# Performance work log

Hardware: AMD Instinct MI355X
Metric: run time of the kernel (lower is better)

## Reference

```python
import jax, jax.numpy as jnp
import numpy as np

N_EMBD = 1024
N_HEAD = 16
LATENT = 64
HEAD_DIM = N_EMBD // N_HEAD
B, T = 2, 2048
SCALE = 1.0 / np.sqrt(LATENT)


def setup_inputs() -> dict:
    key = jax.random.key(0)
    ks = jax.random.split(key, 10)
    s = lambda fan_in: 1.0 / np.sqrt(fan_in)
    return {
        "x": jax.random.normal(ks[0], (B, T, N_EMBD), dtype=jnp.float32),
        "Wq": jax.random.normal(ks[1], (N_EMBD, N_EMBD), dtype=jnp.float32) * s(N_EMBD),
        "bq": jnp.zeros((N_EMBD,), dtype=jnp.float32),
        "Wk": jax.random.normal(ks[2], (N_EMBD, N_HEAD * LATENT), dtype=jnp.float32) * s(N_EMBD),
        "bk": jnp.zeros((N_HEAD * LATENT,), dtype=jnp.float32),
        "Wv": jax.random.normal(ks[3], (N_EMBD, N_HEAD * LATENT), dtype=jnp.float32) * s(N_EMBD),
        "bv": jnp.zeros((N_HEAD * LATENT,), dtype=jnp.float32),
        "Wo": jax.random.normal(ks[4], (N_HEAD * LATENT, N_EMBD), dtype=jnp.float32) * s(N_HEAD * LATENT),
        "bo": jnp.zeros((N_EMBD,), dtype=jnp.float32),
        "Wc": jax.random.normal(ks[5], (HEAD_DIM, LATENT), dtype=jnp.float32) * s(HEAD_DIM),
    }


def reference(x, Wq, bq, Wk, bk, Wv, bv, Wo, bo, Wc):
    Bv, Tv, C = x.shape
    # projections
    q = (x @ Wq + bq).reshape(Bv, Tv, N_HEAD, HEAD_DIM)        # [B,T,H,Dh]
    k = (x @ Wk + bk).reshape(Bv, Tv, N_HEAD, LATENT)          # [B,T,H,L]
    v = (x @ Wv + bv).reshape(Bv, Tv, N_HEAD, LATENT)          # [B,T,H,L]
    # compress q into latent dim: [B,T,H,L]
    qc = jnp.einsum("bthd,dl->bthl", q, Wc)
    # attention scores [B,H,T,T]
    att = jnp.einsum("bthl,bshl->bhts", qc, k) * SCALE
    causal = jnp.tril(jnp.ones((Tv, Tv), dtype=bool))
    att = jnp.where(causal[None, None], att, -jnp.inf)
    att = jax.nn.softmax(att, axis=-1)
    y = jnp.einsum("bhts,bshl->bthl", att, v).reshape(Bv, Tv, N_HEAD * LATENT)
    return y @ Wo + bo
```

## Files before the change

kernel.cpp:

```cpp
#include <hip/hip_runtime.h>
#include <stdint.h>

#define TT 2048
#define BB 2
#define MROWS (BB*TT)
#define LSCALE 0.18033688011112043f

typedef unsigned short u16;
typedef __bf16 bf16x8 __attribute__((ext_vector_type(8)));
typedef float f32x4 __attribute__((ext_vector_type(4)));
typedef short s16x8 __attribute__((ext_vector_type(8)));
typedef unsigned short u16x4 __attribute__((ext_vector_type(4)));

#define GLOBAL_AS const __attribute__((address_space(1))) void*
#define LDS_AS __attribute__((address_space(3))) void*

__device__ __forceinline__ u16 f2b(float f){
  uint32_t u = __builtin_bit_cast(uint32_t, f);
  u = (u + 0x7FFFu + ((u >> 16) & 1u)) >> 16;
  return (u16)u;
}
__device__ __forceinline__ float b2f(u16 u){
  return __builtin_bit_cast(float, (uint32_t)u << 16);
}

__global__ __launch_bounds__(256) void prep(
    const float* __restrict__ x, const float* __restrict__ Wq,
    const float* __restrict__ Wc, const float* __restrict__ bq,
    const float* __restrict__ Wk, const float* __restrict__ Wv,
    const float* __restrict__ Wo,
    u16* __restrict__ xb, u16* __restrict__ WqcT, u16* __restrict__ WkT,
    u16* __restrict__ WvT, u16* __restrict__ WoT, float* __restrict__ bqc){
  const int i = blockIdx.x, t = threadIdx.x;
  if (i < 4096){
    int id = i * 256 + t;
    float4 v = ((const float4*)x)[id];
    u16x4 o; o.x = f2b(v.x); o.y = f2b(v.y); o.z = f2b(v.z); o.w = f2b(v.w);
    ((u16x4*)xb)[id] = o;
    return;
  }
  if (i < 7168){
    int j = i - 4096;
    int z = j >> 10, rem = j & 1023;
    const float* in = (z == 0) ? Wk : (z == 1) ? Wv : Wo;
    u16* out = (z == 0) ? WkT : (z == 1) ? WvT : WoT;
    __shared__ float tl[32][33];
    int tx = t & 31, ty = t >> 5;
    int c0 = (rem & 31) * 32, r0 = (rem >> 5) * 32;
    #pragma unroll
    for (int k = 0; k < 32; k += 8)
      tl[ty + k][tx] = in[(size_t)(r0 + ty + k) * 1024 + c0 + tx];
    __syncthreads();
    #pragma unroll
    for (int k = 0; k < 32; k += 8)
      out[(size_t)(c0 + ty + k) * 1024 + r0 + tx] = f2b(tl[tx][ty + k]);
    return;
  }
  __shared__ float wc[4096];
  #pragma unroll
  for (int k = 0; k < 16; ++k) wc[k * 256 + t] = Wc[k * 256 + t];
  __syncthreads();
  if (i == 7424){
    #pragma unroll
    for (int k = 0; k < 4; ++k){
      int nn = t * 4 + k;
      int h = nn >> 6, lc = nn & 63;
      float a = 0.f;
      #pragma unroll
      for (int dd = 0; dd < 64; ++dd) a += bq[h * 64 + dd] * wc[dd * 64 + lc];
      bqc[nn] = a;
    }
    return;
  }
  __shared__ float tile[64][65];
  const int j = i - 7168;
  const int db = j >> 4, hb = j & 15;
  {
    int dl = t >> 2, lq = t & 3;
    const float4* wq4 = (const float4*)(Wq + (size_t)(db * 64 + dl) * 1024 + hb * 64);
    float wqr[64];
    #pragma unroll
    for (int k = 0; k < 16; ++k){
      float4 v = wq4[k];
      wqr[k * 4] = v.x; wqr[k * 4 + 1] = v.y; wqr[k * 4 + 2] = v.z; wqr[k * 4 + 3] = v.w;
    }
    #pragma unroll
    for (int jj = 0; jj < 16; ++jj){
      int lc = lq * 16 + jj;
      float a = 0.f;
      #pragma unroll
      for (int dd = 0; dd < 64; ++dd) a += wqr[dd] * wc[dd * 64 + lc];
      tile[dl][lc] = a;
    }
  }
  __syncthreads();
  {
    int nl = t >> 2, dq = t & 3;
    u16* dst = WqcT + (size_t)(hb * 64 + nl) * 1024 + db * 64 + dq * 16;
    #pragma unroll
    for (int k = 0; k < 16; ++k)
      dst[k] = f2b(tile[dq * 16 + k][nl]);
  }
}

__global__ void transpose_v(const u16* __restrict__ vb, u16* __restrict__ vt){
  __shared__ u16 t[32][34];
  int tx = threadIdx.x & 31, ty = threadIdx.x >> 5;
  int s0 = blockIdx.x * 32, d0 = blockIdx.y * 32, bh = blockIdx.z;
  int b = bh >> 4, h = bh & 15;
  #pragma unroll
  for (int i = 0; i < 32; i += 8)
    t[ty + i][tx] = vb[(size_t)(b * TT + s0 + ty + i) * 1024 + h * 64 + d0 + tx];
  __syncthreads();
  #pragma unroll
  for (int i = 0; i < 32; i += 8)
    vt[((size_t)bh * 64 + d0 + ty + i) * TT + s0 + tx] = t[tx][ty + i];
}

__device__ __forceinline__ void gemm_tile(const u16* __restrict__ A, const u16* __restrict__ BT,
                                          int m0, int n0, int K, f32x4 (&acc)[4][4],
                                          u16* As, u16* Bs, int tid){
  const int wv = tid >> 6, l = tid & 63;
  const int aoff = ((wv >> 1) * 64 + (l & 15)) * 32 + ((l >> 4) << 3);
  const int boff = ((wv & 1) * 64 + (l & 15)) * 32 + ((l >> 4) << 3);
  const int ob0 = wv * 1024 + l * 16;
  for (int kt = 0; kt < K; kt += 32){
    __syncthreads();
    #pragma unroll
    for (int j = 0; j < 2; ++j){
      int ob = ob0 + j * 4096;
      int row = ob >> 6, col = (ob & 63) >> 1;
      __builtin_amdgcn_global_load_lds((GLOBAL_AS)(A + (size_t)(m0 + row) * 1024 + kt + col),
                                       (LDS_AS)(As + wv * 512 + j * 2048), 16, 0, 0);
      __builtin_amdgcn_global_load_lds((GLOBAL_AS)(BT + (size_t)(n0 + row) * 1024 + kt + col),
                                       (LDS_AS)(Bs + wv * 512 + j * 2048), 16, 0, 0);
    }
    __syncthreads();
    bf16x8 av[4], bw[4];
    #pragma unroll
    for (int m = 0; m < 4; ++m) av[m] = *(const bf16x8*)(As + aoff + m * 512);
    #pragma unroll
    for (int n = 0; n < 4; ++n) bw[n] = *(const bf16x8*)(Bs + boff + n * 512);
    #pragma unroll
    for (int m = 0; m < 4; ++m)
      #pragma unroll
      for (int n = 0; n < 4; ++n)
        acc[m][n] = __builtin_amdgcn_mfma_f32_16x16x32_bf16(av[m], bw[n], acc[m][n], 0, 0, 0);
  }
}

__global__ __launch_bounds__(256) void gemm_qkv(
    const u16* __restrict__ xb,
    const u16* __restrict__ W0T, const u16* __restrict__ W1T, const u16* __restrict__ W2T,
    const float* __restrict__ b0, const float* __restrict__ b1, const float* __restrict__ b2,
    u16* __restrict__ o0, u16* __restrict__ o1, u16* __restrict__ o2){
  __shared__ u16 As[4096], Bs[4096];
  const int z = blockIdx.z;
  const u16* BT = (z == 0) ? W0T : (z == 1) ? W1T : W2T;
  const float* bias = (z == 0) ? b0 : (z == 1) ? b1 : b2;
  u16* Out = (z == 0) ? o0 : (z == 1) ? o1 : o2;
  const float osc = (z == 0) ? LSCALE : 1.0f;
  const int n0 = blockIdx.x * 128, m0 = blockIdx.y * 128;
  const int tid = threadIdx.x, wv = tid >> 6, l = tid & 63;
  f32x4 acc[4][4] = {};
  gemm_tile(xb, BT, m0, n0, 1024, acc, As, Bs, tid);
  const int wr = wv >> 1, wc = wv & 1;
  #pragma unroll
  for (int n = 0; n < 4; ++n){
    int col = n0 + wc * 64 + n * 16 + (l & 15);
    float bb = bias[col];
    #pragma unroll
    for (int m = 0; m < 4; ++m){
      int r0 = m0 + wr * 64 + m * 16 + ((l >> 4) << 2);
      #pragma unroll
      for (int r = 0; r < 4; ++r)
        Out[(size_t)(r0 + r) * 1024 + col] = f2b((acc[m][n][r] + bb) * osc);
    }
  }
}

__global__ __launch_bounds__(256) void gemm_o(
    const u16* __restrict__ A, const u16* __restrict__ BT,
    const float* __restrict__ bias, float* __restrict__ Out){
  __shared__ u16 As[2048], Bs[4096];
  const int n0 = blockIdx.x * 128, m0 = blockIdx.y * 64;
  const int tid = threadIdx.x, wv = tid >> 6, l = tid & 63;
  const int wr = wv >> 1, wc = wv & 1;
  const int aoff = (wr * 32 + (l & 15)) * 32 + ((l >> 4) << 3);
  const int boff = (wc * 64 + (l & 15)) * 32 + ((l >> 4) << 3);
  const int obA = wv * 1024 + l * 16;
  const int rowA = obA >> 6, colA = (obA & 63) >> 1;
  const int ob0 = wv * 1024 + l * 16;
  f32x4 acc[2][4] = {};
  for (int kt = 0; kt < 1024; kt += 32){
    __syncthreads();
    __builtin_amdgcn_global_load_lds((GLOBAL_AS)(A + (size_t)(m0 + rowA) * 1024 + kt + colA),
                                     (LDS_AS)(As + wv * 512), 16, 0, 0);
    #pragma unroll
    for (int j = 0; j < 2; ++j){
      int ob = ob0 + j * 4096;
      int row = ob >> 6, col = (ob & 63) >> 1;
      __builtin_amdgcn_global_load_lds((GLOBAL_AS)(BT + (size_t)(n0 + row) * 1024 + kt + col),
                                       (LDS_AS)(Bs + wv * 512 + j * 2048), 16, 0, 0);
    }
    __syncthreads();
    bf16x8 av[2], bw[4];
    #pragma unroll
    for (int m = 0; m < 2; ++m) av[m] = *(const bf16x8*)(As + aoff + m * 512);
    #pragma unroll
    for (int n = 0; n < 4; ++n) bw[n] = *(const bf16x8*)(Bs + boff + n * 512);
    #pragma unroll
    for (int m = 0; m < 2; ++m)
      #pragma unroll
      for (int n = 0; n < 4; ++n)
        acc[m][n] = __builtin_amdgcn_mfma_f32_16x16x32_bf16(av[m], bw[n], acc[m][n], 0, 0, 0);
  }
  #pragma unroll
  for (int n = 0; n < 4; ++n){
    int col = n0 + wc * 64 + n * 16 + (l & 15);
    float bb = bias[col];
    #pragma unroll
    for (int m = 0; m < 2; ++m){
      int r0 = m0 + wr * 32 + m * 16 + ((l >> 4) << 2);
      #pragma unroll
      for (int r = 0; r < 4; ++r)
        Out[(size_t)(r0 + r) * 1024 + col] = acc[m][n][r] + bb;
    }
  }
}

__device__ const uint8_t gtab[48] = {
  31, 95, 30, 143,  94, 29, 93, 28, 142,  92, 27, 91, 26, 141,
  90, 25, 89, 24, 140,  88, 23, 87, 22, 139,  86, 21, 85, 20, 138,
  84, 19, 83, 18, 137,  82, 17, 81, 16, 136,  80, 135, 134, 133, 132,
  131, 130, 129, 128
};

__global__ __launch_bounds__(256) void attn(
    const u16* __restrict__ qcg, const u16* __restrict__ kg,
    const u16* __restrict__ vtg, u16* __restrict__ yg,
    u16* __restrict__ yp, float* __restrict__ mp, float* __restrict__ lp){
  __shared__ u16 Ks[4096], Vs[4096];
  __shared__ u16 Ps[4096];
  const int idx = blockIdx.x;
  const int g = idx >> 5, bh = idx & 31;
  const int gv_ = gtab[g];
  const int qt = gv_ & 31, piece = gv_ >> 6;
  const int hh = (qt + 2) >> 1;
  const int st0 = (piece == 1) ? hh : 0;
  const int st1 = (piece == 0) ? hh : qt + 1;
  const int pid = (piece == 2) ? -1 : ((31 - qt) * 32 + bh) * 2 + piece;
  const int b = bh >> 4, h = bh & 15;
  const int q0 = qt * 64;
  const int tid = threadIdx.x, wv = tid >> 6, l = tid & 63;
  const int c4 = l >> 4, q16 = l & 15;
  const size_t base = (size_t)b * TT * 1024 + h * 64;
  const u16* Q = qcg + base;
  const u16* K = kg + base;
  const u16* Vt = vtg + (size_t)bh * 64 * TT;

  const int sr = tid >> 3;
  const int sc = (tid & 7) ^ (sr & 7);
  const u16* gK = K + (size_t)sr * 1024 + sc * 8;
  const u16* gV = Vt + (size_t)sr * TT + sc * 8;

  bf16x8 qf[2];
  {
    int qr = q0 + wv * 16 + q16;
    #pragma unroll
    for (int ks = 0; ks < 2; ++ks)
      qf[ks] = *(const bf16x8*)(Q + (size_t)qr * 1024 + ks * 32 + (c4 << 3));
  }
  f32x4 yacc[4] = {};
  float mrow = -1e30f, srow = 0.f;

  uint32_t* const PsW = (uint32_t*)Ps + wv * 512 + q16 * 32;
  const int pm = (q16 & 7) << 2;

  u16* const kd = Ks + wv * 512;
  u16* const vd = Vs + wv * 512;

  for (int st = st0; st < st1; ++st){
    {
      const size_t o = (size_t)st * 64;
      __builtin_amdgcn_global_load_lds((GLOBAL_AS)(gK + o * 1024), (LDS_AS)kd, 16, 0, 0);
      __builtin_amdgcn_global_load_lds((GLOBAL_AS)(gK + (o + 32) * 1024), (LDS_AS)(kd + 2048), 16, 0, 0);
      __builtin_amdgcn_global_load_lds((GLOBAL_AS)(gV + o), (LDS_AS)vd, 16, 0, 0);
      __builtin_amdgcn_global_load_lds((GLOBAL_AS)(gV + o + 32 * TT), (LDS_AS)(vd + 2048), 16, 0, 0);
    }
    asm volatile("s_waitcnt vmcnt(0)" ::: "memory");
    __builtin_amdgcn_sched_barrier(0);
    __builtin_amdgcn_s_barrier();
    __builtin_amdgcn_sched_barrier(0);
    const int s0 = st * 64;
    f32x4 sf[4] = {};
    __builtin_amdgcn_s_setprio(1);
    #pragma unroll
    for (int ks = 0; ks < 2; ++ks)
      #pragma unroll
      for (int nf = 0; nf < 4; ++nf){
        int r = nf * 16 + q16, c = ks * 4 + c4;
        bf16x8 kf = *(const bf16x8*)(Ks + (r * 8 + (c ^ (r & 7))) * 8);
        sf[nf] = __builtin_amdgcn_mfma_f32_16x16x32_bf16(kf, qf[ks], sf[nf], 0, 0, 0);
      }
    __builtin_amdgcn_s_setprio(0);
    const int qa = q0 + wv * 16 + q16;
    float p[4][4];
    const bool domask = (st == qt);
    #pragma unroll
    for (int nf = 0; nf < 4; ++nf)
      #pragma unroll
      for (int r = 0; r < 4; ++r){
        float v_ = sf[nf][r];
        if (domask && (s0 + nf * 16 + c4 * 4 + r > qa)) v_ = -1e30f;
        p[nf][r] = v_;
      }
    float tmax = p[0][0];
    #pragma unroll
    for (int nf = 0; nf < 4; ++nf)
      #pragma unroll
      for (int r = 0; r < 4; ++r) tmax = fmaxf(tmax, p[nf][r]);
    tmax = fmaxf(tmax, __shfl_xor(tmax, 16));
    tmax = fmaxf(tmax, __shfl_xor(tmax, 32));
    if (__any(tmax > mrow + 8.0f)){
      float mnew = fmaxf(mrow, tmax);
      float resc = exp2f(mrow - mnew);
      srow *= resc;
      mrow = mnew;
      #pragma unroll
      for (int df = 0; df < 4; ++df)
        #pragma unroll
        for (int r = 0; r < 4; ++r) yacc[df][r] *= resc;
    }
    float tsum = 0.f;
    #pragma unroll
    for (int nf = 0; nf < 4; ++nf)
      #pragma unroll
      for (int r = 0; r < 4; ++r){ float e = exp2f(p[nf][r] - mrow); p[nf][r] = e; tsum += e; }
    tsum += __shfl_xor(tsum, 16);
    tsum += __shfl_xor(tsum, 32);
    srow += tsum;
    #pragma unroll
    for (int nf = 0; nf < 4; ++nf){
      uint32_t w0, w1;
      asm volatile("v_cvt_pk_bf16_f32 %0, %1, %2" : "=v"(w0) : "v"(p[nf][0]), "v"(p[nf][1]));
      asm volatile("v_cvt_pk_bf16_f32 %0, %1, %2" : "=v"(w1) : "v"(p[nf][2]), "v"(p[nf][3]));
      *(uint64_t*)(PsW + ((nf * 8 + c4 * 2) ^ pm)) = (uint64_t)w0 | ((uint64_t)w1 << 32);
    }
    asm volatile("s_waitcnt lgkmcnt(0)" ::: "memory");
    __builtin_amdgcn_sched_barrier(0);
    __builtin_amdgcn_s_setprio(1);
    #pragma unroll
    for (int ks2 = 0; ks2 < 2; ++ks2){
      bf16x8 pf = *(const bf16x8*)(PsW + ((ks2 * 16 + c4 * 4) ^ pm));
      #pragma unroll
      for (int df = 0; df < 4; ++df){
        int rd = df * 16 + q16, cd = ks2 * 4 + c4;
        bf16x8 vf = *(const bf16x8*)(Vs + (rd * 8 + (cd ^ (rd & 7))) * 8);
        yacc[df] = __builtin_amdgcn_mfma_f32_16x16x32_bf16(vf, pf, yacc[df], 0, 0, 0);
      }
    }
    __builtin_amdgcn_s_setprio(0);
    __builtin_amdgcn_s_barrier();
  }

  if (pid >= 0){
    const int qq = wv * 16 + q16;
    #pragma unroll
    for (int df = 0; df < 4; ++df){
      int d0 = df * 16 + c4 * 4;
      #pragma unroll
      for (int r = 0; r < 4; ++r)
        yp[(size_t)pid * 4096 + qq * 64 + d0 + r] = f2b(yacc[df][r]);
    }
    if (c4 == 0){
      mp[pid * 64 + qq] = mrow;
      lp[pid * 64 + qq] = srow;
    }
  } else {
    const float inv = 1.f / srow;
    const int qq = q0 + wv * 16 + q16;
    #pragma unroll
    for (int df = 0; df < 4; ++df){
      int d0 = df * 16 + c4 * 4;
      #pragma unroll
      for (int r = 0; r < 4; ++r)
        yg[(size_t)(b * TT + qq) * 1024 + h * 64 + d0 + r] = f2b(yacc[df][r] * inv);
    }
  }
}

__global__ __launch_bounds__(256) void attn_combine(
    const u16* __restrict__ yp, const float* __restrict__ mp, const float* __restrict__ lp,
    u16* __restrict__ yg){
  const int cid = blockIdx.x;
  const int qt = 31 - (cid >> 5), bh = cid & 31;
  const int pid0 = cid * 2;
  const int t = threadIdx.x;
  const int q = t >> 2, dc = (t & 3) * 16;
  float m1 = mp[pid0 * 64 + q], m2 = mp[(pid0 + 1) * 64 + q];
  float l1 = lp[pid0 * 64 + q], l2 = lp[(pid0 + 1) * 64 + q];
  float ms = fmaxf(m1, m2);
  float w1 = exp2f(m1 - ms), w2 = exp2f(m2 - ms);
  float inv = 1.f / (l1 * w1 + l2 * w2);
  w1 *= inv; w2 *= inv;
  const int b = bh >> 4, h = bh & 15;
  const s16x8* p1 = (const s16x8*)(yp + (size_t)pid0 * 4096 + q * 64 + dc);
  const s16x8* p2 = (const s16x8*)(yp + (size_t)(pid0 + 1) * 4096 + q * 64 + dc);
  u16* dst = yg + (size_t)(b * TT + qt * 64 + q) * 1024 + h * 64 + dc;
  #pragma unroll
  for (int j2 = 0; j2 < 2; ++j2){
    s16x8 a = p1[j2], c = p2[j2];
    s16x8 o;
    #pragma unroll
    for (int j = 0; j < 8; ++j)
      o[j] = (short)f2b(b2f((u16)a[j]) * w1 + b2f((u16)c[j]) * w2);
    *(s16x8*)(dst + j2 * 8) = o;
  }
}

extern "C" void kernel_launch(void* const* d_in, const int* in_sizes, int n_in,
                              void* d_out, int out_size, void* d_ws, size_t ws_size,
                              hipStream_t stream){
  (void)in_sizes; (void)n_in; (void)out_size; (void)ws_size;
  const float* x  = (const float*)d_in[0];
  const float* Wq = (const float*)d_in[1];
  const float* bq = (const float*)d_in[2];
  const float* Wk = (const float*)d_in[3];
  const float* bk = (const float*)d_in[4];
  const float* Wv = (const float*)d_in[5];
  const float* bv = (const float*)d_in[6];
  const float* Wo = (const float*)d_in[7];
  const float* bo = (const float*)d_in[8];
  const float* Wc = (const float*)d_in[9];
  float* out = (float*)d_out;

  char* wsb = (char*)d_ws;
  u16* xb    = (u16*)(wsb);
  u16* yb    = (u16*)(wsb);
  u16* qcb   = (u16*)(wsb + (8u  << 20));
  u16* kb    = (u16*)(wsb + (16u << 20));
  u16* vb    = (u16*)(wsb + (24u << 20));
  u16* yp    = (u16*)(wsb + (24u << 20));
  u16* vtb   = (u16*)(wsb + (33u << 20));
  float* mp  = (float*)(wsb + (41u << 20));
  float* lp  = (float*)(wsb + (41u << 20) + (1u << 19));
  u16* WqcT  = (u16*)(wsb + (42u << 20));
  u16* WkT   = (u16*)(wsb + (44u << 20));
  u16* WvT   = (u16*)(wsb + (46u << 20));
  u16* WoT   = (u16*)(wsb + (48u << 20));
  float* bqc  = (float*)(wsb + (50u << 20));

  prep<<<7425, 256, 0, stream>>>(x, Wq, Wc, bq, Wk, Wv, Wo,
                                 xb, WqcT, WkT, WvT, WoT, bqc);
  gemm_qkv<<<dim3(8, 32, 3), 256, 0, stream>>>(xb, WqcT, WkT, WvT, bqc, bk, bv, qcb, kb, vb);
  transpose_v<<<dim3(64, 2, 32), 256, 0, stream>>>(vb, vtb);
  attn<<<dim3(1536), 256, 0, stream>>>(qcb, kb, vtb, yb, yp, mp, lp);
  attn_combine<<<dim3(512), 256, 0, stream>>>(yp, mp, lp, yb);
  gemm_o<<<dim3(8, 64), 256, 0, stream>>>(yb, WoT, bo, out);
}
```

Measured before the change: 127.7 us.

## Drop split-KV attention and combine kernel; one block per query tile

Removes the scheme that split the long causal query tiles into two KV pieces with partial outputs, a table-driven schedule and a separate combine kernel. Each block now handles one full query tile, longest first, over all its KV tiles, and writes normalised output directly. This saves one kernel launch and the round trip of partial results through memory. The cost is worse load balance: the longest blocks run up to 32 KV iterations and there are fewer blocks overall.

```diff
diff --git a/kernel.cpp b/kernel.cpp
--- a/kernel.cpp
+++ b/kernel.cpp
@@ -19,9 +19,6 @@
   uint32_t u = __builtin_bit_cast(uint32_t, f);
   u = (u + 0x7FFFu + ((u >> 16) & 1u)) >> 16;
   return (u16)u;
-}
-__device__ __forceinline__ float b2f(u16 u){
-  return __builtin_bit_cast(float, (uint32_t)u << 16);
 }
 
 __global__ __launch_bounds__(256) void prep(
@@ -229,27 +226,13 @@
   }
 }
 
-__device__ const uint8_t gtab[48] = {
-  31, 95, 30, 143,  94, 29, 93, 28, 142,  92, 27, 91, 26, 141,
-  90, 25, 89, 24, 140,  88, 23, 87, 22, 139,  86, 21, 85, 20, 138,
-  84, 19, 83, 18, 137,  82, 17, 81, 16, 136,  80, 135, 134, 133, 132,
-  131, 130, 129, 128
-};
-
 __global__ __launch_bounds__(256) void attn(
     const u16* __restrict__ qcg, const u16* __restrict__ kg,
-    const u16* __restrict__ vtg, u16* __restrict__ yg,
-    u16* __restrict__ yp, float* __restrict__ mp, float* __restrict__ lp){
+    const u16* __restrict__ vtg, u16* __restrict__ yg){
   __shared__ u16 Ks[4096], Vs[4096];
   __shared__ u16 Ps[4096];
   const int idx = blockIdx.x;
-  const int g = idx >> 5, bh = idx & 31;
-  const int gv_ = gtab[g];
-  const int qt = gv_ & 31, piece = gv_ >> 6;
-  const int hh = (qt + 2) >> 1;
-  const int st0 = (piece == 1) ? hh : 0;
-  const int st1 = (piece == 0) ? hh : qt + 1;
-  const int pid = (piece == 2) ? -1 : ((31 - qt) * 32 + bh) * 2 + piece;
+  const int qt = 31 - (idx >> 5), bh = idx & 31;
   const int b = bh >> 4, h = bh & 15;
   const int q0 = qt * 64;
   const int tid = threadIdx.x, wv = tid >> 6, l = tid & 63;
@@ -280,7 +263,8 @@
   u16* const kd = Ks + wv * 512;
   u16* const vd = Vs + wv * 512;
 
-  for (int st = st0; st < st1; ++st){
+  const int nt = qt + 1;
+  for (int st = 0; st < nt; ++st){
     {
       const size_t o = (size_t)st * 64;
       __builtin_amdgcn_global_load_lds((GLOBAL_AS)(gK + o * 1024), (LDS_AS)kd, 16, 0, 0);
@@ -364,58 +348,14 @@
     __builtin_amdgcn_s_barrier();
   }
 
-  if (pid >= 0){
-    const int qq = wv * 16 + q16;
-    #pragma unroll
-    for (int df = 0; df < 4; ++df){
-      int d0 = df * 16 + c4 * 4;
-      #pragma unroll
-      for (int r = 0; r < 4; ++r)
-        yp[(size_t)pid * 4096 + qq * 64 + d0 + r] = f2b(yacc[df][r]);
-    }
-    if (c4 == 0){
-      mp[pid * 64 + qq] = mrow;
-      lp[pid * 64 + qq] = srow;
-    }
-  } else {
-    const float inv = 1.f / srow;
-    const int qq = q0 + wv * 16 + q16;
-    #pragma unroll
-    for (int df = 0; df < 4; ++df){
-      int d0 = df * 16 + c4 * 4;
-      #pragma unroll
-      for (int r = 0; r < 4; ++r)
-        yg[(size_t)(b * TT + qq) * 1024 + h * 64 + d0 + r] = f2b(yacc[df][r] * inv);
-    }
-  }
-}
-
-__global__ __launch_bounds__(256) void attn_combine(
-    const u16* __restrict__ yp, const float* __restrict__ mp, const float* __restrict__ lp,
-    u16* __restrict__ yg){
-  const int cid = blockIdx.x;
-  const int qt = 31 - (cid >> 5), bh = cid & 31;
-  const int pid0 = cid * 2;
-  const int t = threadIdx.x;
-  const int q = t >> 2, dc = (t & 3) * 16;
-  float m1 = mp[pid0 * 64 + q], m2 = mp[(pid0 + 1) * 64 + q];
-  float l1 = lp[pid0 * 64 + q], l2 = lp[(pid0 + 1) * 64 + q];
-  float ms = fmaxf(m1, m2);
-  float w1 = exp2f(m1 - ms), w2 = exp2f(m2 - ms);
-  float inv = 1.f / (l1 * w1 + l2 * w2);
-  w1 *= inv; w2 *= inv;
-  const int b = bh >> 4, h = bh & 15;
-  const s16x8* p1 = (const s16x8*)(yp + (size_t)pid0 * 4096 + q * 64 + dc);
-  const s16x8* p2 = (const s16x8*)(yp + (size_t)(pid0 + 1) * 4096 + q * 64 + dc);
-  u16* dst = yg + (size_t)(b * TT + qt * 64 + q) * 1024 + h * 64 + dc;
-  #pragma unroll
-  for (int j2 = 0; j2 < 2; ++j2){
-    s16x8 a = p1[j2], c = p2[j2];
-    s16x8 o;
-    #pragma unroll
-    for (int j = 0; j < 8; ++j)
-      o[j] = (short)f2b(b2f((u16)a[j]) * w1 + b2f((u16)c[j]) * w2);
-    *(s16x8*)(dst + j2 * 8) = o;
+  const float inv = 1.f / srow;
+  const int qq = q0 + wv * 16 + q16;
+  #pragma unroll
+  for (int df = 0; df < 4; ++df){
+    int d0 = df * 16 + c4 * 4;
+    #pragma unroll
+    for (int r = 0; r < 4; ++r)
+      yg[(size_t)(b * TT + qq) * 1024 + h * 64 + d0 + r] = f2b(yacc[df][r] * inv);
   }
 }
 
@@ -441,10 +381,7 @@
   u16* qcb   = (u16*)(wsb + (8u  << 20));
   u16* kb    = (u16*)(wsb + (16u << 20));
   u16* vb    = (u16*)(wsb + (24u << 20));
-  u16* yp    = (u16*)(wsb + (24u << 20));
   u16* vtb   = (u16*)(wsb + (33u << 20));
-  float* mp  = (float*)(wsb + (41u << 20));
-  float* lp  = (float*)(wsb + (41u << 20) + (1u << 19));
   u16* WqcT  = (u16*)(wsb + (42u << 20));
   u16* WkT   = (u16*)(wsb + (44u << 20));
   u16* WvT   = (u16*)(wsb + (46u << 20));
@@ -455,7 +392,6 @@
                                  xb, WqcT, WkT, WvT, WoT, bqc);
   gemm_qkv<<<dim3(8, 32, 3), 256, 0, stream>>>(xb, WqcT, WkT, WvT, bqc, bk, bv, qcb, kb, vb);
   transpose_v<<<dim3(64, 2, 32), 256, 0, stream>>>(vb, vtb);
-  attn<<<dim3(1536), 256, 0, stream>>>(qcb, kb, vtb, yb, yp, mp, lp);
-  attn_combine<<<dim3(512), 256, 0, stream>>>(yp, mp, lp, yb);
+  attn<<<dim3(1024), 256, 0, stream>>>(qcb, kb, vtb, yb);
   gemm_o<<<dim3(8, 64), 256, 0, stream>>>(yb, WoT, bo, out);
 }
```

After: 125.0 us. -2.1%, faster.
